# Performance work log

Measured on AMD Instinct MI355X. Metric: run time of the kernel, lower is better.

Reference implementation:

```python
import jax, jax.numpy as jnp
import numpy as np

B, N_HEADS, KEY_DIM, ATTN_RATIO, RES, DIM = 8, 12, 64, 4, 32, 768
D = ATTN_RATIO * KEY_DIM          # per-head v dim = 256
DH = N_HEADS * D                  # 3072
QKV_OUT = N_HEADS * (2 * KEY_DIM + D)  # 4608
N = RES * RES                     # 1024 tokens
TH = 0.99
WBITS, ABITS, PGABITS = 8, 8, 4


def quantize(x, bits):
    # TorchQuantize: round(x * 2^(b-1)) / 2^(b-1) with straight-through estimator
    s = jnp.asarray(2.0 ** (bits - 1), x.dtype)
    q = jnp.round(x * s) / s
    return x + jax.lax.stop_gradient(q - x)


def ste_greater_than(x, th):
    # GreaterThan: hard (x > th) forward, identity gradient
    hard = (x > th).astype(x.dtype)
    return x + jax.lax.stop_gradient(hard - x)


def hardswish(x):
    return x * jnp.clip(x + 3.0, 0.0, 6.0) / 6.0


def _make_bias_idxs(res):
    pts = np.stack(np.meshgrid(np.arange(res), np.arange(res), indexing='ij'), -1).reshape(-1, 2)
    off = np.abs(pts[:, None, :] - pts[None, :, :])          # [N,N,2]
    key = off[..., 0] * res + off[..., 1]
    uniq, inv = np.unique(key, return_inverse=True)
    return inv.reshape(res * res, res * res).astype(np.int32), len(uniq)


def setup_inputs() -> dict:
    key = jax.random.key(0)
    ks = jax.random.split(key, 8)
    bias_idxs_np, n_uniq = _make_bias_idxs(RES)
    return {
        "x": jax.random.normal(ks[0], (B, N, DIM), jnp.float32),
        "qkv_w": jax.random.normal(ks[1], (QKV_OUT, DIM), jnp.float32) * (DIM ** -0.5),
        "qkv_g": jnp.ones((QKV_OUT,), jnp.float32),
        "qkv_b": jnp.zeros((QKV_OUT,), jnp.float32),
        "proj_w": jax.random.normal(ks[2], (DIM, DH), jnp.float32) * (DH ** -0.5),
        "proj_g": jnp.ones((DIM,), jnp.float32),
        "proj_b": jnp.zeros((DIM,), jnp.float32),
        "attn_biases": jax.random.normal(ks[3], (N_HEADS, n_uniq), jnp.float32) * 0.02,
        "bias_idxs": jnp.asarray(bias_idxs_np),
    }


def reference(x, qkv_w, qkv_g, qkv_b, proj_w, proj_g, proj_b, attn_biases, bias_idxs):
    Bq, Nq, C = x.shape
    scale = KEY_DIM ** -0.5
    # QLinear qkv (8-bit act/weight) followed by fused BN affine (Linear_BN)
    h = quantize(x, ABITS) @ quantize(qkv_w, WBITS).T
    h = h * qkv_g + qkv_b                                     # [B,N,QKV_OUT]
    h = quantize(h, ABITS)
    h = h.reshape(Bq, Nq, N_HEADS, 2 * KEY_DIM + D).transpose(0, 2, 1, 3)  # [B,H,N,*]
    q, k, v = h[..., :KEY_DIM], h[..., KEY_DIM:2 * KEY_DIM], h[..., 2 * KEY_DIM:]
    bias = attn_biases[:, bias_idxs]                          # [H,N,N]
    # MSB (low-precision) predictive attention -> gating mask
    q_msb = quantize(q, PGABITS)
    k_msb = quantize(k, PGABITS)
    attn_msb = jnp.einsum('bhnd,bhmd->bhnm', q_msb, k_msb) * scale + bias
    attn_msb = jax.nn.softmax(attn_msb, axis=-1)
    mask = ste_greater_than(attn_msb, TH)                     # [B,H,N,N]
    # Full-precision attention, threshold-gated (ena_schedule=False)
    attn = jnp.einsum('bhnd,bhmd->bhnm', q, k) * scale + bias
    attn = jax.nn.softmax(attn * mask, axis=-1)
    attn = quantize(attn, ABITS)
    out = jnp.einsum('bhnm,bhmd->bhnd', attn, v)              # [B,H,N,D]
    out = out.transpose(0, 2, 1, 3).reshape(Bq, Nq, DH)
    out = hardswish(out)                                      # proj = Seq(act, Linear_BN)
    out = quantize(out, ABITS) @ quantize(proj_w, WBITS).T
    out = out * proj_g + proj_b                               # [B,N,DIM]
    return out
```

## Files before the change

kernel.cpp:

```cpp
#include <hip/hip_runtime.h>

typedef _Float16 f16;
typedef _Float16 f16x8 __attribute__((ext_vector_type(8)));
typedef _Float16 f16x4 __attribute__((ext_vector_type(4)));
typedef float    f32x4 __attribute__((ext_vector_type(4)));
typedef int      i32x4 __attribute__((ext_vector_type(4)));

#define MFMA16(a,b,c) __builtin_amdgcn_mfma_f32_16x16x32_f16((a),(b),(c),0,0,0)
#define MFMAI8(a,b,c) __builtin_amdgcn_mfma_i32_16x16x64_i8((a),(b),(c),0,0,0)
#define AS1(p) ((const __attribute__((address_space(1))) void*)(p))
#define AS3(p) ((__attribute__((address_space(3))) void*)(p))

constexpr int   NH   = 12;
constexpr int   SEQ  = 1024;
constexpr float INV128 = 1.0f/128.0f;
constexpr int   ECAP = 98304;
constexpr float THR_NOT = -4.5948f;

__device__ __forceinline__ float q8f(float x){ return rintf(x*128.0f)*INV128; }
__device__ __forceinline__ float q4f(float x){ return rintf(x*8.0f)*0.125f; }

__global__ __launch_bounds__(256) void prelude(
    const float* __restrict__ x, const float* __restrict__ qkv_w,
    float* __restrict__ out, const float* __restrict__ pb,
    const float* __restrict__ biases, int NU,
    f16* __restrict__ xq, f16* __restrict__ wqk, f16* __restrict__ wv,
    float* __restrict__ Bh, int* __restrict__ cnt2)
{
    const int b = blockIdx.x, t = threadIdx.x;
    if (b < 6144){
        int i = (b*256 + t)*4;
        float4 v = *(const float4*)(x + i);
        f16x4 o;
        o[0]=(f16)q8f(v.x); o[1]=(f16)q8f(v.y); o[2]=(f16)q8f(v.z); o[3]=(f16)q8f(v.w);
        *(f16x4*)(xq + i) = o;
    } else if (b < 9600){
        int i = ((b-6144)*256 + t)*4;
        int r = i / 768, col = i - r*768;
        int head = r / 384, rr = r - head*384;
        f16* drow = (rr < 128) ? (wqk + (size_t)(head*128 + rr)*768)
                               : (wv  + (size_t)(head*256 + rr - 128)*768);
        float4 v = *(const float4*)(qkv_w + i);
        f16x4 o;
        o[0]=(f16)q8f(v.x); o[1]=(f16)q8f(v.y); o[2]=(f16)q8f(v.z); o[3]=(f16)q8f(v.w);
        *(f16x4*)(drow + col) = o;
    } else if (b < 15744){
        int i = ((b-9600)*256 + t)*4;
        int c = i % 768;
        float4 v = { pb[c], pb[c+1], pb[c+2], pb[c+3] };
        *(float4*)(out + i) = v;
    } else {
        int h = b - 15744;
        float m = 0.f;
        for (int i = t; i < NU; i += 256) m = fmaxf(m, fabsf(biases[h*NU + i]));
        #pragma unroll
        for (int d=32; d>=1; d>>=1) m = fmaxf(m, __shfl_xor(m, d));
        __shared__ float s[4];
        if ((t&63)==0) s[t>>6] = m;
        __syncthreads();
        if (t==0){
            Bh[h] = fmaxf(fmaxf(s[0],s[1]), fmaxf(s[2],s[3]));
            if (h==0) *cnt2 = 0;
        }
    }
}

__global__ __launch_bounds__(512) void gemm_qk(
    const f16* __restrict__ Aq, const f16* __restrict__ Wqk,
    const float* __restrict__ g, const float* __restrict__ bb,
    signed char* __restrict__ Qi, signed char* __restrict__ Ki)
{
    __shared__ f16 As[2][256][64];
    __shared__ f16 Bs[2][192][64];
    const int t = threadIdx.x;
    const int bid = blockIdx.x;
    const int idx = bid >> 3;
    const int mt  = (bid & 7)*4 + (idx >> 3);
    const int nt  = idx & 7;
    const int row0 = mt*256, col0 = nt*192;
    const int w = t>>6, lane = t&63;
    const int wr = (w>>2)*128, wc = (w&3)*48;
    const int lr = lane&15, lg = lane>>4;

    const int srow  = w*8 + (lane>>3);
    const int sgran = (lane&7) ^ (lane>>3);
    const f16* Abase = Aq  + (size_t)(row0 + srow)*768 + sgran*8;
    const f16* Bbase = Wqk + (size_t)(col0 + srow)*768 + sgran*8;

    f32x4 acc[8][3] = {};

#define STAGE(buf, kt) { \
    const int ko = (kt)*64; \
    __builtin_amdgcn_global_load_lds(AS1(Abase + (size_t)  0*768 + ko), AS3(&As[buf][w*8 +   0][0]), 16, 0, 0); \
    __builtin_amdgcn_global_load_lds(AS1(Abase + (size_t) 64*768 + ko), AS3(&As[buf][w*8 +  64][0]), 16, 0, 0); \
    __builtin_amdgcn_global_load_lds(AS1(Abase + (size_t)128*768 + ko), AS3(&As[buf][w*8 + 128][0]), 16, 0, 0); \
    __builtin_amdgcn_global_load_lds(AS1(Abase + (size_t)192*768 + ko), AS3(&As[buf][w*8 + 192][0]), 16, 0, 0); \
    __builtin_amdgcn_global_load_lds(AS1(Bbase + (size_t)  0*768 + ko), AS3(&Bs[buf][w*8 +   0][0]), 16, 0, 0); \
    __builtin_amdgcn_global_load_lds(AS1(Bbase + (size_t) 64*768 + ko), AS3(&Bs[buf][w*8 +  64][0]), 16, 0, 0); \
    __builtin_amdgcn_global_load_lds(AS1(Bbase + (size_t)128*768 + ko), AS3(&Bs[buf][w*8 + 128][0]), 16, 0, 0); }

    STAGE(0, 0)

    for (int kt = 0; kt < 12; kt++){
        __builtin_amdgcn_s_barrier();
        if (kt < 11){
            STAGE((kt+1)&1, kt+1)
            asm volatile("s_waitcnt vmcnt(7)" ::: "memory");
        } else {
            asm volatile("s_waitcnt vmcnt(0)" ::: "memory");
        }
        __builtin_amdgcn_s_barrier();

        const int bsel = kt & 1;
        #pragma unroll
        for (int kk=0; kk<2; kk++){
            const int slot = ((kk*4 + lg) ^ (lr&7))*8;
            f16x8 af[8], bf[3];
            #pragma unroll
            for (int i=0;i<8;i++)
                af[i] = *(const f16x8*)&As[bsel][wr + i*16 + lr][slot];
            #pragma unroll
            for (int j=0;j<3;j++)
                bf[j] = *(const f16x8*)&Bs[bsel][wc + j*16 + lr][slot];
            #pragma unroll
            for (int i=0;i<8;i++)
                #pragma unroll
                for (int j=0;j<3;j++)
                    acc[i][j] = MFMA16(af[i], bf[j], acc[i][j]);
        }
    }
#undef STAGE

    #pragma unroll
    for (int j=0;j<3;j++){
        int c = col0 + wc + j*16 + lr;
        int head = c >> 7, rr = c & 127;
        int gcol = head*384 + rr;
        float gg = g[gcol], bv = bb[gcol];
        signed char* dst = (rr < 64) ? Qi : Ki;
        int dcol = rr & 63;
        #pragma unroll
        for (int i=0;i<8;i++){
            #pragma unroll
            for (int r=0;r<4;r++){
                int grow = row0 + wr + i*16 + lg*4 + r;
                float h = __fadd_rn(__fmul_rn(acc[i][j][r], gg), bv);
                int iv = (int)rintf(q8f(h)*8.0f);
                int bq = grow >> 10, n = grow & 1023;
                dst[((size_t)(bq*NH + head)*SEQ + n)*64 + dcol] = (signed char)iv;
            }
        }
    }
}

__global__ __launch_bounds__(256) void pass_a(
    const signed char* __restrict__ Qi, const signed char* __restrict__ Ki,
    const float* __restrict__ Bh,
    int* __restrict__ cnt2, int2* __restrict__ amb)
{
    __shared__ signed char Ks[128][64];

    const int t = threadIdx.x;
    const int bid = blockIdx.x;
    const int wg  = (bid & 7)*192 + (bid >> 3);
    const int bh  = wg >> 4;
    const int qt  = wg & 15;
    const int n0 = qt*64;
    const int lane = t&63, w = t>>6;
    const int lr = lane&15, lg = lane>>4;

    const float thr512 = (THR_NOT + 2.0f*Bh[bh % NH] + 1e-4f) * 512.0f;

    const signed char* qp = Qi + ((size_t)bh*SEQ + n0 + w*16 + lr)*64;
    const i32x4 aq = *(const i32x4*)(qp + lg*16);

    const signed char* Kb = Ki + (size_t)bh*SEQ*64;

    int mx[4], m2[4];
    #pragma unroll
    for (int r=0;r<4;r++){ mx[r] = -(1<<30); m2[r] = -(1<<30); }

    for (int kb = 0; kb < SEQ; kb += 128){
        __syncthreads();
        for (int s = t; s < 512; s += 256){
            int r = s>>2, gsw = s&3;
            int src = (gsw ^ (r&3))*16;
            *(i32x4*)&Ks[r][gsw*16] = *(const i32x4*)(Kb + (size_t)(kb + r)*64 + src);
        }
        __syncthreads();
        #pragma unroll
        for (int ct=0; ct<8; ct++){
            const int row = ct*16 + lr;
            i32x4 bq = *(const i32x4*)&Ks[row][(lg ^ (lr&3))*16];
            i32x4 c = {0,0,0,0};
            c = MFMAI8(aq, bq, c);
            #pragma unroll
            for (int r=0;r<4;r++){
                int sc = c[r];
                int om = mx[r];
                m2[r] = max(m2[r], min(sc, om));
                mx[r] = max(om, sc);
            }
        }
    }

    #pragma unroll
    for (int r=0;r<4;r++){
        int mxv = mx[r], m2v = m2[r];
        #pragma unroll
        for (int d=1; d<16; d<<=1){
            int mo  = __shfl_xor(mxv, d);
            int m2o = __shfl_xor(m2v, d);
            int sec = max(min(mxv, mo), (mxv >= mo) ? m2v : m2o);
            mxv = max(mxv, mo);
            m2v = sec;
        }
        if (lr == 0){
            if ((float)(m2v - mxv) < thr512){
                int n = n0 + w*16 + lg*4 + r;
                int pos = atomicAdd(cnt2, 1);
                if (pos < ECAP) amb[pos] = make_int2((bh<<10) | n, 0);
            }
        }
    }
}

__global__ __launch_bounds__(256) void tail_kernel(
    const signed char* __restrict__ Qi, const signed char* __restrict__ Ki,
    const float* __restrict__ biases, int NU,
    const f16* __restrict__ xq, const f16* __restrict__ wqk, const f16* __restrict__ wv,
    const float* __restrict__ g, const float* __restrict__ bb,
    const float* __restrict__ proj_w, const float* __restrict__ pg,
    const int* __restrict__ cnt2, const int2* __restrict__ amb,
    float* __restrict__ out)
{
    __shared__ int   qr[64];
    __shared__ float rmax[4], rsum[4];
    __shared__ int   rarg[4];
    __shared__ float xr_n[768], xr_m[768];
    __shared__ float qs[64], ks[64];
    __shared__ float hq[256];
    __shared__ float s_as;
    __shared__ int   s_ms, s_flag;
    int total = *cnt2; if (total > ECAP) total = ECAP;
    const int t = threadIdx.x;
    for (int e = blockIdx.x; e < total; e += gridDim.x){
        int2 a = amb[e];
        int bh = a.x>>10, n = a.x&1023;
        int h = bh % NH, b = bh / NH;
        __syncthreads();
        if (t < 64) qr[t] = (int)Qi[((size_t)bh*SEQ + n)*64 + t];
        __syncthreads();

        int rn = n>>5, cnn = n&31;
        float lmax = -3e38f; int larg = 0; float lsc[4];
        #pragma unroll
        for (int j=0;j<4;j++){
            int m = t + j*256;
            const signed char* kp = &Ki[((size_t)bh*SEQ + m)*64];
            int d = 0;
            for (int u=0; u<64; u++) d += qr[u]*(int)kp[u];
            int idx = __builtin_abs(rn-(m>>5))*32 + __builtin_abs(cnn-(m&31));
            lsc[j] = (float)d*(1.0f/512.0f) + biases[h*NU + idx];
            if (lsc[j] > lmax){ lmax = lsc[j]; larg = m; }
        }
        #pragma unroll
        for (int dd=32; dd>=1; dd>>=1){
            float mo = __shfl_xor(lmax, dd);
            int   ao = __shfl_xor(larg, dd);
            if (mo > lmax){ lmax = mo; larg = ao; }
        }
        if ((t&63)==0){ rmax[t>>6] = lmax; rarg[t>>6] = larg; }
        __syncthreads();
        float MX = rmax[0]; int ARG = rarg[0];
        #pragma unroll
        for (int k=1;k<4;k++){ if (rmax[k] > MX){ MX = rmax[k]; ARG = rarg[k]; } }
        float ls = 0.f;
        #pragma unroll
        for (int j=0;j<4;j++) ls += expf(lsc[j]-MX);
        #pragma unroll
        for (int dd=32; dd>=1; dd>>=1) ls += __shfl_xor(ls, dd);
        if ((t&63)==0) rsum[t>>6] = ls;
        __syncthreads();
        if (t==0){
            float SUM = rsum[0]+rsum[1]+rsum[2]+rsum[3];
            s_flag = (1.0f/SUM > 0.99f);
            s_ms = ARG;
        }
        __syncthreads();
        if (!s_flag) continue;
        const int ms = s_ms;

        for (int i=t; i<768; i+=256){
            xr_n[i] = (float)xq[((size_t)b*SEQ + n)*768 + i];
            xr_m[i] = (float)xq[((size_t)b*SEQ + ms)*768 + i];
        }
        __syncthreads();
        if (t < 128){
            int col = t & 63;
            int qkr  = h*128 + (t<64 ? col : 64+col);
            int gcol = h*384 + (t<64 ? col : 64+col);
            const f16* wr = &wqk[(size_t)qkr*768];
            const float* xr = (t<64) ? xr_n : xr_m;
            float acc = 0.f;
            for (int d=0; d<768; d++) acc = fmaf(xr[d], (float)wr[d], acc);
            float hv = __fadd_rn(__fmul_rn(acc, g[gcol]), bb[gcol]);
            float v = q8f(hv);
            if (t<64) qs[col] = v; else ks[col] = v;
        }
        __syncthreads();
        if (t < 64){
            float p = qs[t]*ks[t];
            #pragma unroll
            for (int d=32; d>=1; d>>=1) p += __shfl_xor(p, d);
            if (t == 0){
                int idx = __builtin_abs((n>>5)-(ms>>5))*32 + __builtin_abs((n&31)-(ms&31));
                float ss = __fadd_rn(__fmul_rn(p, 0.125f), biases[h*NU + idx]);
                float mx2 = fmaxf(ss, 0.f);
                float es = expf(ss-mx2), e0 = expf(-mx2);
                float Z = fmaf(1023.f, e0, es);
                s_as = q8f(es/Z);
            }
        }
        __syncthreads();
        {
            int gcol = h*384 + 128 + t;
            const f16* wr = &wv[(size_t)(h*256 + t)*768];
            float acc = 0.f;
            for (int d=0; d<768; d++) acc = fmaf(xr_m[d], (float)wr[d], acc);
            float hv = __fadd_rn(__fmul_rn(acc, g[gcol]), bb[gcol]);
            float vq = q8f(hv);
            float o = __fmul_rn(s_as, vq);
            float c6 = fminf(fmaxf(o+3.f, 0.f), 6.f);
            hq[t] = q8f(__fdiv_rn(__fmul_rn(o, c6), 6.f));
        }
        __syncthreads();
        #pragma unroll
        for (int cc=0; cc<3; cc++){
            int c = t + cc*256;
            float s = 0.f;
            for (int d=0; d<256; d++)
                s = fmaf(hq[d], q8f(proj_w[(size_t)c*3072 + h*256 + d]), s);
            atomicAdd(&out[((size_t)b*SEQ + n)*768 + c], __fmul_rn(pg[c], s));
        }
    }
}

extern "C" void kernel_launch(void* const* d_in, const int* in_sizes, int n_in,
                              void* d_out, int out_size, void* d_ws, size_t ws_size,
                              hipStream_t stream)
{
    const float* x       = (const float*)d_in[0];
    const float* qkv_w   = (const float*)d_in[1];
    const float* qkv_g   = (const float*)d_in[2];
    const float* qkv_b   = (const float*)d_in[3];
    const float* proj_w  = (const float*)d_in[4];
    const float* proj_g  = (const float*)d_in[5];
    const float* proj_b  = (const float*)d_in[6];
    const float* biases  = (const float*)d_in[7];
    const int NU = in_sizes[7] / NH;

    char* w = (char*)d_ws;
    f16* xq  = (f16*)w; w += (size_t)8192*768*2;
    f16* wqk = (f16*)w; w += (size_t)1536*768*2;
    f16* wv  = (f16*)w; w += (size_t)3072*768*2;
    signed char* Qi = (signed char*)w; w += (size_t)96*1024*64;
    signed char* Ki = (signed char*)w; w += (size_t)96*1024*64;
    int* cnt2= (int*)w;  w += 16;
    float* Bh = (float*)w; w += 64;
    int2* amb = (int2*)w; w += (size_t)ECAP*8;

    prelude<<<15756, 256, 0, stream>>>(x, qkv_w, (float*)d_out, proj_b, biases, NU,
                                       xq, wqk, wv, Bh, cnt2);

    gemm_qk<<<256, 512, 0, stream>>>(xq, wqk, qkv_g, qkv_b, Qi, Ki);

    pass_a<<<1536, 256, 0, stream>>>(Qi, Ki, Bh, cnt2, amb);

    tail_kernel<<<256, 256, 0, stream>>>(Qi, Ki, biases, NU, xq, wqk, wv,
                                         qkv_g, qkv_b, proj_w, proj_g,
                                         cnt2, amb, (float*)d_out);
}
```

Baseline: 62.96 us.

## Shrink QK GEMM tiles, drop V weight pre-conversion, use med3 in pass_a

The prelude no longer converts the V slice of qkv_w to fp16. Only the Q/K rows are quantized, gathered directly from the interleaved layout, and tail_kernel reads fp32 V weights and quantizes them on the fly. gemm_qk moves from 256x192 tiles with 512 threads to 128x192 tiles with 256 threads and two blocks per CU, and raises MFMA priority with setprio. pass_a's running second-max update becomes a single v_med3_i32. The aim is less prelude traffic and better GEMM occupancy, at the cost of extra quantize work per element in the sparse tail path.

```diff
diff --git a/kernel.cpp b/kernel.cpp
--- a/kernel.cpp
+++ b/kernel.cpp
@@ -24,7 +24,7 @@
     const float* __restrict__ x, const float* __restrict__ qkv_w,
     float* __restrict__ out, const float* __restrict__ pb,
     const float* __restrict__ biases, int NU,
-    f16* __restrict__ xq, f16* __restrict__ wqk, f16* __restrict__ wv,
+    f16* __restrict__ xq, f16* __restrict__ wqk,
     float* __restrict__ Bh, int* __restrict__ cnt2)
 {
     const int b = blockIdx.x, t = threadIdx.x;
@@ -34,23 +34,21 @@
         f16x4 o;
         o[0]=(f16)q8f(v.x); o[1]=(f16)q8f(v.y); o[2]=(f16)q8f(v.z); o[3]=(f16)q8f(v.w);
         *(f16x4*)(xq + i) = o;
-    } else if (b < 9600){
+    } else if (b < 7296){
         int i = ((b-6144)*256 + t)*4;
         int r = i / 768, col = i - r*768;
-        int head = r / 384, rr = r - head*384;
-        f16* drow = (rr < 128) ? (wqk + (size_t)(head*128 + rr)*768)
-                               : (wv  + (size_t)(head*256 + rr - 128)*768);
-        float4 v = *(const float4*)(qkv_w + i);
+        int srow = (r>>7)*384 + (r&127);
+        float4 v = *(const float4*)(qkv_w + (size_t)srow*768 + col);
         f16x4 o;
         o[0]=(f16)q8f(v.x); o[1]=(f16)q8f(v.y); o[2]=(f16)q8f(v.z); o[3]=(f16)q8f(v.w);
-        *(f16x4*)(drow + col) = o;
-    } else if (b < 15744){
-        int i = ((b-9600)*256 + t)*4;
+        *(f16x4*)(wqk + i) = o;
+    } else if (b < 13440){
+        int i = ((b-7296)*256 + t)*4;
         int c = i % 768;
         float4 v = { pb[c], pb[c+1], pb[c+2], pb[c+3] };
         *(float4*)(out + i) = v;
     } else {
-        int h = b - 15744;
+        int h = b - 13440;
         float m = 0.f;
         for (int i = t; i < NU; i += 256) m = fmaxf(m, fabsf(biases[h*NU + i]));
         #pragma unroll
@@ -65,39 +63,42 @@
     }
 }
 
-__global__ __launch_bounds__(512) void gemm_qk(
+__global__ __launch_bounds__(256, 2) void gemm_qk(
     const f16* __restrict__ Aq, const f16* __restrict__ Wqk,
     const float* __restrict__ g, const float* __restrict__ bb,
     signed char* __restrict__ Qi, signed char* __restrict__ Ki)
 {
-    __shared__ f16 As[2][256][64];
+    __shared__ f16 As[2][128][64];
     __shared__ f16 Bs[2][192][64];
     const int t = threadIdx.x;
     const int bid = blockIdx.x;
-    const int idx = bid >> 3;
-    const int mt  = (bid & 7)*4 + (idx >> 3);
+    const int xcd = bid & 7, idx = bid >> 3;
+    const int mt  = xcd*8 + (idx >> 3);
     const int nt  = idx & 7;
-    const int row0 = mt*256, col0 = nt*192;
+    const int row0 = mt*128, col0 = nt*192;
     const int w = t>>6, lane = t&63;
-    const int wr = (w>>2)*128, wc = (w&3)*48;
+    const int wr = (w>>1)*64, wc = (w&1)*96;
     const int lr = lane&15, lg = lane>>4;
 
-    const int srow  = w*8 + (lane>>3);
-    const int sgran = (lane&7) ^ (lane>>3);
-    const f16* Abase = Aq  + (size_t)(row0 + srow)*768 + sgran*8;
-    const f16* Bbase = Wqk + (size_t)(col0 + srow)*768 + sgran*8;
-
-    f32x4 acc[8][3] = {};
+    const int rloc  = lane>>3;
+    const int sgran = (lane&7) ^ rloc;
+    const f16* Abase = Aq  + (size_t)(row0 + w*32 + rloc)*768 + sgran*8;
+    const f16* Bbase = Wqk + (size_t)(col0 + w*48 + rloc)*768 + sgran*8;
+
+    f32x4 acc[4][6] = {};
 
 #define STAGE(buf, kt) { \
     const int ko = (kt)*64; \
-    __builtin_amdgcn_global_load_lds(AS1(Abase + (size_t)  0*768 + ko), AS3(&As[buf][w*8 +   0][0]), 16, 0, 0); \
-    __builtin_amdgcn_global_load_lds(AS1(Abase + (size_t) 64*768 + ko), AS3(&As[buf][w*8 +  64][0]), 16, 0, 0); \
-    __builtin_amdgcn_global_load_lds(AS1(Abase + (size_t)128*768 + ko), AS3(&As[buf][w*8 + 128][0]), 16, 0, 0); \
-    __builtin_amdgcn_global_load_lds(AS1(Abase + (size_t)192*768 + ko), AS3(&As[buf][w*8 + 192][0]), 16, 0, 0); \
-    __builtin_amdgcn_global_load_lds(AS1(Bbase + (size_t)  0*768 + ko), AS3(&Bs[buf][w*8 +   0][0]), 16, 0, 0); \
-    __builtin_amdgcn_global_load_lds(AS1(Bbase + (size_t) 64*768 + ko), AS3(&Bs[buf][w*8 +  64][0]), 16, 0, 0); \
-    __builtin_amdgcn_global_load_lds(AS1(Bbase + (size_t)128*768 + ko), AS3(&Bs[buf][w*8 + 128][0]), 16, 0, 0); }
+    __builtin_amdgcn_global_load_lds(AS1(Abase + (size_t) 0*768 + ko), AS3(&As[buf][w*32 +  0][0]), 16, 0, 0); \
+    __builtin_amdgcn_global_load_lds(AS1(Abase + (size_t) 8*768 + ko), AS3(&As[buf][w*32 +  8][0]), 16, 0, 0); \
+    __builtin_amdgcn_global_load_lds(AS1(Abase + (size_t)16*768 + ko), AS3(&As[buf][w*32 + 16][0]), 16, 0, 0); \
+    __builtin_amdgcn_global_load_lds(AS1(Abase + (size_t)24*768 + ko), AS3(&As[buf][w*32 + 24][0]), 16, 0, 0); \
+    __builtin_amdgcn_global_load_lds(AS1(Bbase + (size_t) 0*768 + ko), AS3(&Bs[buf][w*48 +  0][0]), 16, 0, 0); \
+    __builtin_amdgcn_global_load_lds(AS1(Bbase + (size_t) 8*768 + ko), AS3(&Bs[buf][w*48 +  8][0]), 16, 0, 0); \
+    __builtin_amdgcn_global_load_lds(AS1(Bbase + (size_t)16*768 + ko), AS3(&Bs[buf][w*48 + 16][0]), 16, 0, 0); \
+    __builtin_amdgcn_global_load_lds(AS1(Bbase + (size_t)24*768 + ko), AS3(&Bs[buf][w*48 + 24][0]), 16, 0, 0); \
+    __builtin_amdgcn_global_load_lds(AS1(Bbase + (size_t)32*768 + ko), AS3(&Bs[buf][w*48 + 32][0]), 16, 0, 0); \
+    __builtin_amdgcn_global_load_lds(AS1(Bbase + (size_t)40*768 + ko), AS3(&Bs[buf][w*48 + 40][0]), 16, 0, 0); }
 
     STAGE(0, 0)
 
@@ -105,7 +106,7 @@
         __builtin_amdgcn_s_barrier();
         if (kt < 11){
             STAGE((kt+1)&1, kt+1)
-            asm volatile("s_waitcnt vmcnt(7)" ::: "memory");
+            asm volatile("s_waitcnt vmcnt(10)" ::: "memory");
         } else {
             asm volatile("s_waitcnt vmcnt(0)" ::: "memory");
         }
@@ -115,24 +116,26 @@
         #pragma unroll
         for (int kk=0; kk<2; kk++){
             const int slot = ((kk*4 + lg) ^ (lr&7))*8;
-            f16x8 af[8], bf[3];
-            #pragma unroll
-            for (int i=0;i<8;i++)
+            f16x8 af[4], bf[6];
+            #pragma unroll
+            for (int i=0;i<4;i++)
                 af[i] = *(const f16x8*)&As[bsel][wr + i*16 + lr][slot];
             #pragma unroll
-            for (int j=0;j<3;j++)
+            for (int j=0;j<6;j++)
                 bf[j] = *(const f16x8*)&Bs[bsel][wc + j*16 + lr][slot];
-            #pragma unroll
-            for (int i=0;i<8;i++)
+            __builtin_amdgcn_s_setprio(1);
+            #pragma unroll
+            for (int i=0;i<4;i++)
                 #pragma unroll
-                for (int j=0;j<3;j++)
+                for (int j=0;j<6;j++)
                     acc[i][j] = MFMA16(af[i], bf[j], acc[i][j]);
+            __builtin_amdgcn_s_setprio(0);
         }
     }
 #undef STAGE
 
     #pragma unroll
-    for (int j=0;j<3;j++){
+    for (int j=0;j<6;j++){
         int c = col0 + wc + j*16 + lr;
         int head = c >> 7, rr = c & 127;
         int gcol = head*384 + rr;
@@ -140,7 +143,7 @@
         signed char* dst = (rr < 64) ? Qi : Ki;
         int dcol = rr & 63;
         #pragma unroll
-        for (int i=0;i<8;i++){
+        for (int i=0;i<4;i++){
             #pragma unroll
             for (int r=0;r<4;r++){
                 int grow = row0 + wr + i*16 + lg*4 + r;
@@ -198,7 +201,7 @@
             for (int r=0;r<4;r++){
                 int sc = c[r];
                 int om = mx[r];
-                m2[r] = max(m2[r], min(sc, om));
+                asm("v_med3_i32 %0, %1, %2, %3" : "=v"(m2[r]) : "v"(sc), "v"(m2[r]), "v"(om));
                 mx[r] = max(om, sc);
             }
         }
@@ -228,7 +231,8 @@
 __global__ __launch_bounds__(256) void tail_kernel(
     const signed char* __restrict__ Qi, const signed char* __restrict__ Ki,
     const float* __restrict__ biases, int NU,
-    const f16* __restrict__ xq, const f16* __restrict__ wqk, const f16* __restrict__ wv,
+    const f16* __restrict__ xq, const f16* __restrict__ wqk,
+    const float* __restrict__ qkv_w,
     const float* __restrict__ g, const float* __restrict__ bb,
     const float* __restrict__ proj_w, const float* __restrict__ pg,
     const int* __restrict__ cnt2, const int2* __restrict__ amb,
@@ -325,9 +329,9 @@
         __syncthreads();
         {
             int gcol = h*384 + 128 + t;
-            const f16* wr = &wv[(size_t)(h*256 + t)*768];
+            const float* wr = &qkv_w[(size_t)gcol*768];
             float acc = 0.f;
-            for (int d=0; d<768; d++) acc = fmaf(xr_m[d], (float)wr[d], acc);
+            for (int d=0; d<768; d++) acc = fmaf(xr_m[d], q8f(wr[d]), acc);
             float hv = __fadd_rn(__fmul_rn(acc, g[gcol]), bb[gcol]);
             float vq = q8f(hv);
             float o = __fmul_rn(s_as, vq);
@@ -363,21 +367,20 @@
     char* w = (char*)d_ws;
     f16* xq  = (f16*)w; w += (size_t)8192*768*2;
     f16* wqk = (f16*)w; w += (size_t)1536*768*2;
-    f16* wv  = (f16*)w; w += (size_t)3072*768*2;
     signed char* Qi = (signed char*)w; w += (size_t)96*1024*64;
     signed char* Ki = (signed char*)w; w += (size_t)96*1024*64;
     int* cnt2= (int*)w;  w += 16;
     float* Bh = (float*)w; w += 64;
     int2* amb = (int2*)w; w += (size_t)ECAP*8;
 
-    prelude<<<15756, 256, 0, stream>>>(x, qkv_w, (float*)d_out, proj_b, biases, NU,
-                                       xq, wqk, wv, Bh, cnt2);
-
-    gemm_qk<<<256, 512, 0, stream>>>(xq, wqk, qkv_g, qkv_b, Qi, Ki);
+    prelude<<<13452, 256, 0, stream>>>(x, qkv_w, (float*)d_out, proj_b, biases, NU,
+                                       xq, wqk, Bh, cnt2);
+
+    gemm_qk<<<512, 256, 0, stream>>>(xq, wqk, qkv_g, qkv_b, Qi, Ki);
 
     pass_a<<<1536, 256, 0, stream>>>(Qi, Ki, Bh, cnt2, amb);
 
-    tail_kernel<<<256, 256, 0, stream>>>(Qi, Ki, biases, NU, xq, wqk, wv,
+    tail_kernel<<<256, 256, 0, stream>>>(Qi, Ki, biases, NU, xq, wqk, qkv_w,
                                          qkv_g, qkv_b, proj_w, proj_g,
                                          cnt2, amb, (float*)d_out);
 }
```

Result: faster. 57.27 us (-9.0%).
